# Optimization experiments

Hardware: AMD Instinct MI355X
Metric: run time of the kernel (lower is better)

## Reference

```python
import jax, jax.numpy as jnp
import numpy as np
import math

B, N, D = 8, 4096, 1024
H = 8          # num_heads
NC = 2         # n_classes


def setup_inputs() -> dict:
    key = jax.random.key(0)
    ks = jax.random.split(key, 12)
    s = 1.0 / math.sqrt(D)
    return {
        "inputs": jax.random.normal(ks[0], (B, N, D), jnp.float32),
        # enc: Linear(D, 1) + Sigmoid
        "W_enc": jax.random.normal(ks[1], (1, D), jnp.float32) * s,
        "b_enc": jnp.zeros((1,), jnp.float32),
        "cls_token": jax.random.normal(ks[2], (1, 1, D), jnp.float32) * s,
        # depthwise Conv2d(D, D, 3, padding=1, groups=D)
        "conv_w": jax.random.normal(ks[3], (D, 1, 3, 3), jnp.float32) * 0.1,
        "conv_b": jnp.zeros((D,), jnp.float32),
        # MAB projections (torch Linear weight layout [out, in])
        "Wq": jax.random.normal(ks[4], (D, D), jnp.float32) * s,
        "bq": jnp.zeros((D,), jnp.float32),
        "Wk": jax.random.normal(ks[5], (D, D), jnp.float32) * s,
        "bk": jnp.zeros((D,), jnp.float32),
        "Wv": jax.random.normal(ks[6], (D, D), jnp.float32) * s,
        "bv": jnp.zeros((D,), jnp.float32),
        "Wo": jax.random.normal(ks[7], (D, D), jnp.float32) * s,
        "bo": jnp.zeros((D,), jnp.float32),
        # final classifier Linear(D, NC)
        "Wfc": jax.random.normal(ks[8], (NC, D), jnp.float32) * s,
        "bfc": jnp.zeros((NC,), jnp.float32),
    }


def reference(inputs, W_enc, b_enc, cls_token, conv_w, conv_b,
              Wq, bq, Wk, bk, Wv, bv, Wo, bo, Wfc, bfc):
    b, n, d = inputs.shape
    # ---- recalib(option='max', k=1): top-1 instance per bag as query ----
    a1 = jax.nn.sigmoid(inputs @ W_enc.T + b_enc)[..., 0]            # [B, N]
    idx = jnp.argmax(a1, axis=1)                                      # [B]
    Q = jnp.take_along_axis(inputs, idx[:, None, None], axis=1)       # [B, 1, D]
    # ---- shift_feature ----
    inputs = jax.nn.relu(inputs - Q)
    # ---- pad to square grid, prepend cls token ----
    _H = int(np.ceil(np.sqrt(n)))
    add = _H * _H - n
    x = jnp.concatenate([inputs, inputs[:, :add, :]], axis=1)         # [B, _H*_H, D]
    cls = jnp.broadcast_to(cls_token, (b, 1, d))
    x = jnp.concatenate([cls, x], axis=1)                             # [B, S, D]
    cls_tok, feat = x[:, 0], x[:, 1:]
    # ---- depthwise conv residual on the 2D grid ----
    cnn = feat.transpose(0, 2, 1).reshape(b, d, _H, _H)               # [B, C, H, W]
    conv = jax.lax.conv_general_dilated(
        cnn, conv_w, window_strides=(1, 1), padding='SAME',
        dimension_numbers=('NCHW', 'OIHW', 'NCHW'),
        feature_group_count=d) + conv_b[None, :, None, None]
    cnn = conv + cnn
    xf = cnn.reshape(b, d, _H * _H).transpose(0, 2, 1)
    x = jnp.concatenate([cls_tok[:, None, :], xf], axis=1)            # [B, S, D]
    # ---- MAB(Q, x): manual multi-head attention ----
    Qp = Q @ Wq.T + bq                                                # [B, 1, D]
    K = x @ Wk.T + bk                                                 # [B, S, D]
    V = x @ Wv.T + bv
    dh = d // H
    qh = Qp.reshape(b, 1, H, dh).transpose(0, 2, 1, 3)                # [B, H, 1, dh]
    kh = K.reshape(b, -1, H, dh).transpose(0, 2, 1, 3)                # [B, H, S, dh]
    vh = V.reshape(b, -1, H, dh).transpose(0, 2, 1, 3)
    # NOTE: original scales by sqrt(dim_V), not sqrt(d_head)
    logits = jnp.einsum('bhqd,bhkd->bhqk', qh, kh) / jnp.asarray(math.sqrt(d), jnp.float32)
    A = jax.nn.softmax(logits, axis=-1)
    oh = qh + jnp.einsum('bhqk,bhkd->bhqd', A, vh)                    # residual inside heads
    O = oh.transpose(0, 2, 1, 3).reshape(b, 1, d)                     # [B, 1, D]
    O = O + jax.nn.relu(O @ Wo.T + bo)
    bag = O[:, 0]                                                     # [B, D]
    out = bag @ Wfc.T + bfc                                           # [B, NC]
    return out
```

## Files before the change

kernel.cpp:

```cpp
#include <hip/hip_runtime.h>
#include <hip/hip_bf16.h>


#define NTOK 4096
#define DD 1024

#define FO_ARG 0
#define FO_S1  16
#define FO_CWT 4160
#define FO_QP  13376
#define FO_W   21568
#define FO_MS  87232
#define FO_YP  95424
#define FO_Y   4289728
#define FO_O1  4355264
#define FO_O2  4363456
#define FO_AW  4371648
#define FO_XF  8388608

#define LSTRIDE 101

__global__ void k_init(const float* __restrict__ convw, float* __restrict__ cwT) {
  int gid = blockIdx.x * 256 + threadIdx.x;
  if (gid < 9216) {
    int d = gid / 9, p = gid - d * 9;
    cwT[p * DD + d] = convw[gid];
  }
}

__global__ void k_argmax1(const float* __restrict__ inp, const float* __restrict__ Wenc,
                          const float* __restrict__ benc, unsigned long long* __restrict__ s1buf) {
  __shared__ unsigned long long lb[4];
  int wave = threadIdx.x >> 6, lane = threadIdx.x & 63;
  int b = blockIdx.x >> 8;
  int r0 = ((blockIdx.x & 255) << 4) + (wave << 2);
  const float4* base = (const float4*)(inp + ((size_t)b * NTOK + r0) * DD);
  const float4* wp = (const float4*)Wenc;
  float s0 = 0.f, s1 = 0.f, s2 = 0.f, s3 = 0.f;
#pragma unroll
  for (int k = 0; k < 4; ++k) {
    int off = lane + (k << 6);
    float4 w4 = wp[off];
    float4 a0 = base[off];
    float4 a1 = base[256 + off];
    float4 a2 = base[512 + off];
    float4 a3 = base[768 + off];
    s0 = fmaf(w4.x, a0.x, s0); s0 = fmaf(w4.y, a0.y, s0); s0 = fmaf(w4.z, a0.z, s0); s0 = fmaf(w4.w, a0.w, s0);
    s1 = fmaf(w4.x, a1.x, s1); s1 = fmaf(w4.y, a1.y, s1); s1 = fmaf(w4.z, a1.z, s1); s1 = fmaf(w4.w, a1.w, s1);
    s2 = fmaf(w4.x, a2.x, s2); s2 = fmaf(w4.y, a2.y, s2); s2 = fmaf(w4.z, a2.z, s2); s2 = fmaf(w4.w, a2.w, s2);
    s3 = fmaf(w4.x, a3.x, s3); s3 = fmaf(w4.y, a3.y, s3); s3 = fmaf(w4.z, a3.z, s3); s3 = fmaf(w4.w, a3.w, s3);
  }
#pragma unroll
  for (int mk = 32; mk >= 1; mk >>= 1) {
    s0 += __shfl_xor(s0, mk); s1 += __shfl_xor(s1, mk);
    s2 += __shfl_xor(s2, mk); s3 += __shfl_xor(s3, mk);
  }
  if (lane == 0) {
    float be = benc[0];
    float v[4] = {s0 + be, s1 + be, s2 + be, s3 + be};
    unsigned long long bst = 0ull;
#pragma unroll
    for (int i = 0; i < 4; ++i) {
      unsigned u = __float_as_uint(v[i]);
      u = (u & 0x80000000u) ? ~u : (u | 0x80000000u);
      unsigned long long p = ((unsigned long long)u << 32) |
                             (unsigned long long)(0xFFFFFFFFu - (unsigned)(r0 + i));
      bst = bst > p ? bst : p;
    }
    lb[wave] = bst;
  }
  __syncthreads();
  if (threadIdx.x == 0) {
    unsigned long long m = lb[0];
#pragma unroll
    for (int i = 1; i < 4; ++i) m = m > lb[i] ? m : lb[i];
    s1buf[blockIdx.x] = m;
  }
}

__global__ void k_argmax2(const unsigned long long* __restrict__ s1buf,
                          unsigned long long* __restrict__ argbest) {
  __shared__ unsigned long long red[256];
  int tid = threadIdx.x, b = blockIdx.x;
  red[tid] = s1buf[b * 256 + tid];
  __syncthreads();
  for (int s = 128; s > 0; s >>= 1) {
    if (tid < s) { unsigned long long o = red[tid + s]; if (o > red[tid]) red[tid] = o; }
    __syncthreads();
  }
  if (tid == 0) argbest[b] = red[0];
}

__global__ void k_qp(const float* __restrict__ inp, const float* __restrict__ Wq,
                     const float* __restrict__ bq, const unsigned long long* __restrict__ argbest,
                     float* __restrict__ Qp) {
  int wave = threadIdx.x >> 6, lane = threadIdx.x & 63;
  int b = blockIdx.x >> 8;
  int i = ((blockIdx.x & 255) << 2) + wave;
  unsigned idx = 0xFFFFFFFFu - (unsigned)(argbest[b] & 0xFFFFFFFFull);
  const float4* qr = (const float4*)(inp + ((size_t)b * NTOK + idx) * DD);
  const float4* wr = (const float4*)(Wq + (size_t)i * DD);
  float s = 0.f;
#pragma unroll
  for (int k = 0; k < 4; ++k) {
    float4 a = wr[lane + (k << 6)], x = qr[lane + (k << 6)];
    s = fmaf(a.x, x.x, s); s = fmaf(a.y, x.y, s);
    s = fmaf(a.z, x.z, s); s = fmaf(a.w, x.w, s);
  }
  for (int m = 32; m > 0; m >>= 1) s += __shfl_xor(s, m);
  if (lane == 0) Qp[b * DD + i] = s + bq[i];
}

__global__ void k_w(const float* __restrict__ Wk, const float* __restrict__ Qp,
                    float* __restrict__ wbuf) {
  __shared__ float qs[1024];
  __shared__ float sred[2048];
  const int tid = threadIdx.x;
  const int h = blockIdx.x >> 5, jb = blockIdx.x & 31;
  {
    int b = tid >> 5, i4 = tid & 31;
    ((float4*)qs)[b * 32 + i4] = ((const float4*)Qp)[b * 256 + (h << 5) + i4];
  }
  __syncthreads();
  const int jl = tid & 31, ig = tid >> 5;
  const float* wkp = Wk + (size_t)((h << 7) + (ig << 4)) * DD + (jb << 5) + jl;
  float acc[8];
#pragma unroll
  for (int b = 0; b < 8; ++b) acc[b] = 0.f;
#pragma unroll
  for (int ii = 0; ii < 16; ++ii) {
    float wv = wkp[(size_t)ii * DD];
    int i = (ig << 4) + ii;
#pragma unroll
    for (int b = 0; b < 8; ++b) acc[b] = fmaf(qs[(b << 7) + i], wv, acc[b]);
  }
#pragma unroll
  for (int b = 0; b < 8; ++b) sred[ig * 256 + (b << 5) + jl] = acc[b];
  __syncthreads();
  {
    int b = tid >> 5, j2 = tid & 31;
    float s = 0.f;
#pragma unroll
    for (int g = 0; g < 8; ++g) s += sred[g * 256 + (b << 5) + j2];
    wbuf[(size_t)((b << 3) + h) * DD + (jb << 5) + j2] = s;
  }
}

__global__ __launch_bounds__(512, 4) void k_logits(
    const float* __restrict__ inp, const float* __restrict__ convb,
    const float* __restrict__ cwT, const float* __restrict__ wbuf,
    const unsigned long long* __restrict__ argbest,
    float* __restrict__ plog, float* __restrict__ xf) {
  __shared__ float4 sred4[32 * LSTRIDE];
  const int tid = threadIdx.x, bx = blockIdx.x;
  const int b = bx >> 9, tile = (bx >> 3) & 63, cidx = bx & 7;
  const int R0 = (tile >> 3) << 3, C0 = (tile & 7) << 3;
  const unsigned idxq = 0xFFFFFFFFu - (unsigned)(argbest[b] & 0xFFFFFFFFull);
  const float* inpb = inp + (size_t)b * NTOK * DD;
  const float* qrow = inpb + (size_t)idxq * DD;
  const int gg = tid & 31, ts = tid >> 5;
  const int jg = tid >> 5, rq = (tid >> 3) & 3, ca = tid & 7;
  const int r0a = rq << 1;
  const int jc = cidx << 7;

  float acc[2][8];
#pragma unroll
  for (int i = 0; i < 2; ++i)
#pragma unroll
    for (int h = 0; h < 8; ++h) acc[i][h] = 0.f;
  float4 xs0[2], xs1[2];

  {
    const int js = jc + (gg << 2);
    float4 qv = *(const float4*)(qrow + js);
    for (int t = ts; t < 100; t += 16) {
      int tr = t / 10, tc = t - tr * 10;
      int gr = R0 - 1 + tr, gc = C0 - 1 + tc;
      float4 v = make_float4(0.f, 0.f, 0.f, 0.f);
      if (gr >= 0 && gr < 64 && gc >= 0 && gc < 64) {
        float4 rv = *(const float4*)(inpb + (size_t)((gr << 6) + gc) * DD + js);
        v.x = fmaxf(rv.x - qv.x, 0.f); v.y = fmaxf(rv.y - qv.y, 0.f);
        v.z = fmaxf(rv.z - qv.z, 0.f); v.w = fmaxf(rv.w - qv.w, 0.f);
      }
      sred4[gg * LSTRIDE + t] = v;
    }
  }
  __syncthreads();
#pragma unroll
  for (int sub = 0; sub < 2; ++sub) {
    const int g = (sub << 4) + jg;
    const int j4 = jc + (g << 2);
    float4 cwr[9];
#pragma unroll
    for (int p = 0; p < 9; ++p) cwr[p] = *(const float4*)(cwT + p * DD + j4);
    float4 cb4 = *(const float4*)(convb + j4);
    const float4* fb = sred4 + g * LSTRIDE;
    float4 x0 = cb4, x1 = cb4;
    {
      float4 rw[4][3];
#pragma unroll
      for (int rr = 0; rr < 4; ++rr)
#pragma unroll
        for (int dc = 0; dc < 3; ++dc)
          rw[rr][dc] = fb[(r0a + rr) * 10 + ca + dc];
#pragma unroll
      for (int dr = 0; dr < 3; ++dr)
#pragma unroll
        for (int dc = 0; dc < 3; ++dc) {
          float4 w = cwr[dr * 3 + dc];
          float4 f0 = rw[dr][dc], f1 = rw[dr + 1][dc];
          x0.x = fmaf(w.x, f0.x, x0.x); x0.y = fmaf(w.y, f0.y, x0.y);
          x0.z = fmaf(w.z, f0.z, x0.z); x0.w = fmaf(w.w, f0.w, x0.w);
          x1.x = fmaf(w.x, f1.x, x1.x); x1.y = fmaf(w.y, f1.y, x1.y);
          x1.z = fmaf(w.z, f1.z, x1.z); x1.w = fmaf(w.w, f1.w, x1.w);
        }
      x0.x += rw[1][1].x; x0.y += rw[1][1].y; x0.z += rw[1][1].z; x0.w += rw[1][1].w;
      x1.x += rw[2][1].x; x1.y += rw[2][1].y; x1.z += rw[2][1].z; x1.w += rw[2][1].w;
    }
    xs0[sub] = x0; xs1[sub] = x1;
#pragma unroll
    for (int h = 0; h < 8; ++h) {
      float4 whv = *(const float4*)(wbuf + (size_t)(b * 8 + h) * DD + j4);
      float a0 = acc[0][h], a1 = acc[1][h];
      a0 = fmaf(whv.x, x0.x, a0); a0 = fmaf(whv.y, x0.y, a0);
      a0 = fmaf(whv.z, x0.z, a0); a0 = fmaf(whv.w, x0.w, a0);
      a1 = fmaf(whv.x, x1.x, a1); a1 = fmaf(whv.y, x1.y, a1);
      a1 = fmaf(whv.z, x1.z, a1); a1 = fmaf(whv.w, x1.w, a1);
      acc[0][h] = a0; acc[1][h] = a1;
    }
  }
  __syncthreads();
  float* red = (float*)sred4;
#pragma unroll
  for (int it = 0; it < 2; ++it)
#pragma unroll
    for (int h = 0; h < 8; ++h)
      red[jg * 512 + ((r0a + it) * 8 + ca) * 8 + h] = acc[it][h];
  __syncthreads();
  {
    float s = 0.f;
#pragma unroll
    for (int g = 0; g < 16; ++g) s += red[g * 512 + tid];
    plog[(size_t)bx * 512 + tid] = s;
  }
  __syncthreads();
  float4* ldsx = sred4;
  {
    const int tk0 = (r0a << 3) + ca;
#pragma unroll
    for (int sub = 0; sub < 2; ++sub) {
      int q = (sub << 4) + jg;
      ldsx[tk0 * 33 + q] = xs0[sub];
      ldsx[(tk0 + 8) * 33 + q] = xs1[sub];
    }
  }
  __syncthreads();
  {
    float* xfb = xf + (size_t)((b << 6) + tile) * (64 * DD) + jc;
#pragma unroll
    for (int it = 0; it < 4; ++it) {
      int idx = (it << 9) + tid;
      int tk = idx >> 5, q = idx & 31;
      float4 v = ldsx[tk * 33 + q];
      *(float4*)(xfb + (size_t)tk * DD + (q << 2)) = v;
    }
  }
}

__global__ void k_sm(const float* __restrict__ plog, float* __restrict__ aw,
                     float2* __restrict__ msbuf) {
  __shared__ float atile[512];
  const int tid = threadIdx.x, bt = blockIdx.x;
  const float* pp = plog + (size_t)bt * 8 * 512;
  float s0 = 0.f, s1 = 0.f;
#pragma unroll
  for (int c = 0; c < 8; ++c) {
    s0 += pp[c * 512 + tid];
    s1 += pp[c * 512 + 256 + tid];
  }
  {
    int o = tid, h = o & 7, tok = o >> 3;
    atile[h * 64 + tok] = s0 * 0.03125f;
    o = tid + 256; h = o & 7; tok = o >> 3;
    atile[h * 64 + tok] = s1 * 0.03125f;
  }
  __syncthreads();
  const int hh = tid >> 5, sl = tid & 31;
  float l1 = atile[hh * 64 + sl], l2 = atile[hh * 64 + 32 + sl];
  float mx = fmaxf(l1, l2);
#pragma unroll
  for (int mk = 16; mk >= 1; mk >>= 1) mx = fmaxf(mx, __shfl_xor(mx, mk));
  float e1 = __expf(l1 - mx), e2 = __expf(l2 - mx);
  float Ssum = e1 + e2;
#pragma unroll
  for (int mk = 16; mk >= 1; mk >>= 1) Ssum += __shfl_xor(Ssum, mk);
  aw[(size_t)bt * 512 + sl * 8 + hh] = e1;
  aw[(size_t)bt * 512 + (32 + sl) * 8 + hh] = e2;
  if (sl == 0) {
    int b = bt >> 6, tile = bt & 63;
    msbuf[((b << 3) + hh) * 64 + tile] = make_float2(mx, Ssum);
  }
}

__global__ __launch_bounds__(512, 8) void k_ysum(
    const float* __restrict__ xf, const float* __restrict__ aw,
    float* __restrict__ ypart) {
  __shared__ float atile[512];
  const int tid = threadIdx.x, bt = blockIdx.x;
  atile[tid] = aw[(size_t)bt * 512 + tid];
  __syncthreads();
  const float* xbase = xf + (size_t)bt * (64 * DD) + (tid << 1);
  float2 acc[8];
#pragma unroll
  for (int h = 0; h < 8; ++h) acc[h] = make_float2(0.f, 0.f);
#pragma unroll 4
  for (int t = 0; t < 64; ++t) {
    float2 v = *(const float2*)(xbase + (size_t)t * DD);
    float4 aA = *(const float4*)&atile[t * 8];
    float4 aB = *(const float4*)&atile[t * 8 + 4];
    acc[0].x = fmaf(aA.x, v.x, acc[0].x); acc[0].y = fmaf(aA.x, v.y, acc[0].y);
    acc[1].x = fmaf(aA.y, v.x, acc[1].x); acc[1].y = fmaf(aA.y, v.y, acc[1].y);
    acc[2].x = fmaf(aA.z, v.x, acc[2].x); acc[2].y = fmaf(aA.z, v.y, acc[2].y);
    acc[3].x = fmaf(aA.w, v.x, acc[3].x); acc[3].y = fmaf(aA.w, v.y, acc[3].y);
    acc[4].x = fmaf(aB.x, v.x, acc[4].x); acc[4].y = fmaf(aB.x, v.y, acc[4].y);
    acc[5].x = fmaf(aB.y, v.x, acc[5].x); acc[5].y = fmaf(aB.y, v.y, acc[5].y);
    acc[6].x = fmaf(aB.z, v.x, acc[6].x); acc[6].y = fmaf(aB.z, v.y, acc[6].y);
    acc[7].x = fmaf(aB.w, v.x, acc[7].x); acc[7].y = fmaf(aB.w, v.y, acc[7].y);
  }
  const int b = bt >> 6, tile = bt & 63;
#pragma unroll
  for (int h = 0; h < 8; ++h)
    *(float2*)(ypart + ((size_t)((b * 8 + h) * 64 + tile)) * DD + (tid << 1)) = acc[h];
}

__global__ void k_comb(const float2* __restrict__ msbuf, const float* __restrict__ wbuf,
                       const float* __restrict__ cls, const float* __restrict__ ypart,
                       float* __restrict__ ybuf) {
  __shared__ float redl[256];
  __shared__ float wgt[64];
  __shared__ float wclss;
  __shared__ float4 sacc[256];
  int tid = threadIdx.x;
  int bh = blockIdx.x >> 3, cs = blockIdx.x & 7;
  {
    float4 a = ((const float4*)(wbuf + (size_t)bh * DD))[tid];
    float4 c = ((const float4*)cls)[tid];
    redl[tid] = a.x * c.x + a.y * c.y + a.z * c.z + a.w * c.w;
  }
  __syncthreads();
  for (int s = 128; s > 0; s >>= 1) { if (tid < s) redl[tid] += redl[tid + s]; __syncthreads(); }
  float l0 = redl[0] * 0.03125f;
  if (tid < 64) {
    float2 ms = msbuf[bh * 64 + tid];
    float m = ms.x, S = ms.y;
    float M = m;
#pragma unroll
    for (int mk = 32; mk >= 1; mk >>= 1) M = fmaxf(M, __shfl_xor(M, mk));
    M = fmaxf(M, l0);
    float w = __expf(m - M);
    float z = S * w;
#pragma unroll
    for (int mk = 32; mk >= 1; mk >>= 1) z += __shfl_xor(z, mk);
    float ec = __expf(l0 - M);
    float Z = z + ec;
    wgt[tid] = w / Z;
    if (tid == 0) wclss = ec / Z;
  }
  __syncthreads();
  int ch4 = (cs << 5) + (tid & 31);
  int tg = tid >> 5;
  const float* yp = ypart + (size_t)bh * 64 * DD + (ch4 << 2);
  float4 acc = make_float4(0.f, 0.f, 0.f, 0.f);
#pragma unroll
  for (int tt = 0; tt < 8; ++tt) {
    int t = tg * 8 + tt;
    float w = wgt[t];
    float4 v = *(const float4*)(yp + (size_t)t * DD);
    acc.x = fmaf(w, v.x, acc.x); acc.y = fmaf(w, v.y, acc.y);
    acc.z = fmaf(w, v.z, acc.z); acc.w = fmaf(w, v.w, acc.w);
  }
  sacc[tg * 32 + (tid & 31)] = acc;
  __syncthreads();
  if (tid < 32) {
    int c4 = (cs << 5) + tid;
    float4 s = sacc[tid];
#pragma unroll
    for (int g = 1; g < 8; ++g) {
      float4 v = sacc[g * 32 + tid];
      s.x += v.x; s.y += v.y; s.z += v.z; s.w += v.w;
    }
    float wc = wclss;
    float4 cv = *(const float4*)(cls + (c4 << 2));
    s.x = fmaf(wc, cv.x, s.x); s.y = fmaf(wc, cv.y, s.y);
    s.z = fmaf(wc, cv.z, s.z); s.w = fmaf(wc, cv.w, s.w);
    *(float4*)(ybuf + (size_t)bh * DD + (c4 << 2)) = s;
  }
}

__global__ void k_o1(const float* __restrict__ Wv, const float* __restrict__ bv,
                     const float* __restrict__ Qp, const float* __restrict__ ybuf,
                     float* __restrict__ O1) {
  int wave = threadIdx.x >> 6, lane = threadIdx.x & 63;
  int b = blockIdx.x >> 8;
  int i = ((blockIdx.x & 255) << 2) + wave;
  int h = i >> 7;
  const float4* wr = (const float4*)(Wv + (size_t)i * DD);
  const float4* yr = (const float4*)(ybuf + (size_t)(b * 8 + h) * DD);
  float s = 0.f;
#pragma unroll
  for (int k = 0; k < 4; ++k) {
    float4 a = wr[lane + (k << 6)], x = yr[lane + (k << 6)];
    s = fmaf(a.x, x.x, s); s = fmaf(a.y, x.y, s);
    s = fmaf(a.z, x.z, s); s = fmaf(a.w, x.w, s);
  }
  for (int m = 32; m > 0; m >>= 1) s += __shfl_xor(s, m);
  if (lane == 0) O1[b * DD + i] = Qp[b * DD + i] + bv[i] + s;
}

__global__ void k_o2(const float* __restrict__ Wo, const float* __restrict__ bo,
                     const float* __restrict__ O1, float* __restrict__ O2) {
  int wave = threadIdx.x >> 6, lane = threadIdx.x & 63;
  int b = blockIdx.x >> 8;
  int i = ((blockIdx.x & 255) << 2) + wave;
  const float4* wr = (const float4*)(Wo + (size_t)i * DD);
  const float4* xr = (const float4*)(O1 + (size_t)b * DD);
  float s = 0.f;
#pragma unroll
  for (int k = 0; k < 4; ++k) {
    float4 a = wr[lane + (k << 6)], x = xr[lane + (k << 6)];
    s = fmaf(a.x, x.x, s); s = fmaf(a.y, x.y, s);
    s = fmaf(a.z, x.z, s); s = fmaf(a.w, x.w, s);
  }
  for (int m = 32; m > 0; m >>= 1) s += __shfl_xor(s, m);
  if (lane == 0) O2[b * DD + i] = O1[b * DD + i] + fmaxf(s + bo[i], 0.f);
}

__global__ void k_out(const float* __restrict__ Wfc, const float* __restrict__ bfc,
                      const float* __restrict__ O2, float* __restrict__ out) {
  int wave = threadIdx.x >> 6, lane = threadIdx.x & 63;
  for (int p = wave; p < 16; p += 4) {
    int b = p >> 1, cc = p & 1;
    const float4* o = (const float4*)(O2 + (size_t)b * DD);
    const float4* wr = (const float4*)(Wfc + (size_t)cc * DD);
    float s = 0.f;
#pragma unroll
    for (int k = 0; k < 4; ++k) {
      float4 a = o[lane + (k << 6)], x = wr[lane + (k << 6)];
      s = fmaf(a.x, x.x, s); s = fmaf(a.y, x.y, s);
      s = fmaf(a.z, x.z, s); s = fmaf(a.w, x.w, s);
    }
    for (int m = 32; m > 0; m >>= 1) s += __shfl_xor(s, m);
    if (lane == 0) out[p] = s + bfc[cc];
  }
}

extern "C" void kernel_launch(void* const* d_in, const int* in_sizes, int n_in,
                              void* d_out, int out_size, void* d_ws, size_t ws_size,
                              hipStream_t stream) {
  const float* inp   = (const float*)d_in[0];
  const float* Wenc  = (const float*)d_in[1];
  const float* benc  = (const float*)d_in[2];
  const float* cls   = (const float*)d_in[3];
  const float* convw = (const float*)d_in[4];
  const float* convb = (const float*)d_in[5];
  const float* Wq    = (const float*)d_in[6];
  const float* bq    = (const float*)d_in[7];
  const float* Wk    = (const float*)d_in[8];
  const float* bv    = (const float*)d_in[11];
  const float* Wv    = (const float*)d_in[10];
  const float* Wo    = (const float*)d_in[12];
  const float* bo    = (const float*)d_in[13];
  const float* Wfc   = (const float*)d_in[14];
  const float* bfc   = (const float*)d_in[15];
  float* out = (float*)d_out;
  float* W = (float*)d_ws;
  unsigned long long* argbest = (unsigned long long*)(W + FO_ARG);
  unsigned long long* s1buf   = (unsigned long long*)(W + FO_S1);
  float* cwT   = W + FO_CWT;
  float* Qp    = W + FO_QP;
  float* wbuf  = W + FO_W;
  float2* msbuf = (float2*)(W + FO_MS);
  float* ypart = W + FO_YP;
  float* plog  = W + FO_YP;
  float* aw    = W + FO_AW;
  float* xf    = W + FO_XF;
  float* ybuf  = W + FO_Y;
  float* O1    = W + FO_O1;
  float* O2    = W + FO_O2;

  hipLaunchKernelGGL(k_init,    dim3(36),   dim3(256), 0, stream, convw, cwT);
  hipLaunchKernelGGL(k_argmax1, dim3(2048), dim3(256), 0, stream, inp, Wenc, benc, s1buf);
  hipLaunchKernelGGL(k_argmax2, dim3(8),    dim3(256), 0, stream, s1buf, argbest);
  hipLaunchKernelGGL(k_qp,      dim3(2048), dim3(256), 0, stream, inp, Wq, bq, argbest, Qp);
  hipLaunchKernelGGL(k_w,       dim3(256),  dim3(256), 0, stream, Wk, Qp, wbuf);
  hipLaunchKernelGGL(k_logits,  dim3(4096), dim3(512), 0, stream, inp, convb, cwT, wbuf, argbest, plog, xf);
  hipLaunchKernelGGL(k_sm,      dim3(512),  dim3(256), 0, stream, plog, aw, msbuf);
  hipLaunchKernelGGL(k_ysum,    dim3(512),  dim3(512), 0, stream, xf, aw, ypart);
  hipLaunchKernelGGL(k_comb,    dim3(512),  dim3(256), 0, stream, msbuf, wbuf, cls, ypart, ybuf);
  hipLaunchKernelGGL(k_o1,      dim3(2048), dim3(256), 0, stream, Wv, bv, Qp, ybuf, O1);
  hipLaunchKernelGGL(k_o2,      dim3(2048), dim3(256), 0, stream, Wo, bo, O1, O2);
  hipLaunchKernelGGL(k_out,     dim3(1),    dim3(256), 0, stream, Wfc, bfc, O2, out);
}
```

Measured before the change: 358.3 us.

## Split logits kernel into narrower channel chunks and fuse softmax into ysum

The logits/conv kernel now has each block handle 64 channels instead of 128, which doubles the grid to 8192 blocks and halves per-thread registers and LDS use. The separate softmax kernel is removed: k_ysum now reduces the 16 partial logit slices, computes the per-tile softmax max and sum, and keeps the exp weights in LDS, so the aw buffer round trip and one launch go away. In exchange, the partial-logit buffer doubles in size and moves to a new workspace offset. The halo load per block is also repeated for twice as many blocks.

```diff
diff --git a/kernel.cpp b/kernel.cpp
--- a/kernel.cpp
+++ b/kernel.cpp
@@ -15,8 +15,8 @@
 #define FO_Y   4289728
 #define FO_O1  4355264
 #define FO_O2  4363456
-#define FO_AW  4371648
 #define FO_XF  8388608
+#define FO_PL  41943040
 
 #define LSTRIDE 101
 
@@ -151,29 +151,29 @@
     const float* __restrict__ cwT, const float* __restrict__ wbuf,
     const unsigned long long* __restrict__ argbest,
     float* __restrict__ plog, float* __restrict__ xf) {
-  __shared__ float4 sred4[32 * LSTRIDE];
+  __shared__ float4 sred4[2048];
   const int tid = threadIdx.x, bx = blockIdx.x;
-  const int b = bx >> 9, tile = (bx >> 3) & 63, cidx = bx & 7;
+  const int b = bx >> 10, tile = (bx >> 4) & 63, cidx = bx & 15;
   const int R0 = (tile >> 3) << 3, C0 = (tile & 7) << 3;
   const unsigned idxq = 0xFFFFFFFFu - (unsigned)(argbest[b] & 0xFFFFFFFFull);
   const float* inpb = inp + (size_t)b * NTOK * DD;
   const float* qrow = inpb + (size_t)idxq * DD;
-  const int gg = tid & 31, ts = tid >> 5;
+  const int gg = tid & 15, ts = tid >> 4;
   const int jg = tid >> 5, rq = (tid >> 3) & 3, ca = tid & 7;
   const int r0a = rq << 1;
-  const int jc = cidx << 7;
+  const int jc = cidx << 6;
 
   float acc[2][8];
 #pragma unroll
   for (int i = 0; i < 2; ++i)
 #pragma unroll
     for (int h = 0; h < 8; ++h) acc[i][h] = 0.f;
-  float4 xs0[2], xs1[2];
+  float4 xs0, xs1;
 
   {
     const int js = jc + (gg << 2);
     float4 qv = *(const float4*)(qrow + js);
-    for (int t = ts; t < 100; t += 16) {
+    for (int t = ts; t < 100; t += 32) {
       int tr = t / 10, tc = t - tr * 10;
       int gr = R0 - 1 + tr, gc = C0 - 1 + tc;
       float4 v = make_float4(0.f, 0.f, 0.f, 0.f);
@@ -186,15 +186,13 @@
     }
   }
   __syncthreads();
-#pragma unroll
-  for (int sub = 0; sub < 2; ++sub) {
-    const int g = (sub << 4) + jg;
-    const int j4 = jc + (g << 2);
+  {
+    const int j4 = jc + (jg << 2);
     float4 cwr[9];
 #pragma unroll
     for (int p = 0; p < 9; ++p) cwr[p] = *(const float4*)(cwT + p * DD + j4);
     float4 cb4 = *(const float4*)(convb + j4);
-    const float4* fb = sred4 + g * LSTRIDE;
+    const float4* fb = sred4 + jg * LSTRIDE;
     float4 x0 = cb4, x1 = cb4;
     {
       float4 rw[4][3];
@@ -217,7 +215,7 @@
       x0.x += rw[1][1].x; x0.y += rw[1][1].y; x0.z += rw[1][1].z; x0.w += rw[1][1].w;
       x1.x += rw[2][1].x; x1.y += rw[2][1].y; x1.z += rw[2][1].z; x1.w += rw[2][1].w;
     }
-    xs0[sub] = x0; xs1[sub] = x1;
+    xs0 = x0; xs1 = x1;
 #pragma unroll
     for (int h = 0; h < 8; ++h) {
       float4 whv = *(const float4*)(wbuf + (size_t)(b * 8 + h) * DD + j4);
@@ -247,67 +245,52 @@
   float4* ldsx = sred4;
   {
     const int tk0 = (r0a << 3) + ca;
-#pragma unroll
-    for (int sub = 0; sub < 2; ++sub) {
-      int q = (sub << 4) + jg;
-      ldsx[tk0 * 33 + q] = xs0[sub];
-      ldsx[(tk0 + 8) * 33 + q] = xs1[sub];
-    }
+    ldsx[tk0 * 17 + jg] = xs0;
+    ldsx[(tk0 + 8) * 17 + jg] = xs1;
   }
   __syncthreads();
   {
     float* xfb = xf + (size_t)((b << 6) + tile) * (64 * DD) + jc;
 #pragma unroll
-    for (int it = 0; it < 4; ++it) {
+    for (int it = 0; it < 2; ++it) {
       int idx = (it << 9) + tid;
-      int tk = idx >> 5, q = idx & 31;
-      float4 v = ldsx[tk * 33 + q];
+      int tk = idx >> 4, q = idx & 15;
+      float4 v = ldsx[tk * 17 + q];
       *(float4*)(xfb + (size_t)tk * DD + (q << 2)) = v;
     }
   }
 }
 
-__global__ void k_sm(const float* __restrict__ plog, float* __restrict__ aw,
-                     float2* __restrict__ msbuf) {
+__global__ __launch_bounds__(512, 8) void k_ysum(
+    const float* __restrict__ plog, const float* __restrict__ xf,
+    float2* __restrict__ msbuf, float* __restrict__ ypart) {
   __shared__ float atile[512];
   const int tid = threadIdx.x, bt = blockIdx.x;
-  const float* pp = plog + (size_t)bt * 8 * 512;
-  float s0 = 0.f, s1 = 0.f;
-#pragma unroll
-  for (int c = 0; c < 8; ++c) {
-    s0 += pp[c * 512 + tid];
-    s1 += pp[c * 512 + 256 + tid];
-  }
-  {
-    int o = tid, h = o & 7, tok = o >> 3;
-    atile[h * 64 + tok] = s0 * 0.03125f;
-    o = tid + 256; h = o & 7; tok = o >> 3;
-    atile[h * 64 + tok] = s1 * 0.03125f;
-  }
-  __syncthreads();
-  const int hh = tid >> 5, sl = tid & 31;
-  float l1 = atile[hh * 64 + sl], l2 = atile[hh * 64 + 32 + sl];
-  float mx = fmaxf(l1, l2);
-#pragma unroll
-  for (int mk = 16; mk >= 1; mk >>= 1) mx = fmaxf(mx, __shfl_xor(mx, mk));
-  float e1 = __expf(l1 - mx), e2 = __expf(l2 - mx);
-  float Ssum = e1 + e2;
-#pragma unroll
-  for (int mk = 16; mk >= 1; mk >>= 1) Ssum += __shfl_xor(Ssum, mk);
-  aw[(size_t)bt * 512 + sl * 8 + hh] = e1;
-  aw[(size_t)bt * 512 + (32 + sl) * 8 + hh] = e2;
-  if (sl == 0) {
-    int b = bt >> 6, tile = bt & 63;
-    msbuf[((b << 3) + hh) * 64 + tile] = make_float2(mx, Ssum);
-  }
-}
-
-__global__ __launch_bounds__(512, 8) void k_ysum(
-    const float* __restrict__ xf, const float* __restrict__ aw,
-    float* __restrict__ ypart) {
-  __shared__ float atile[512];
-  const int tid = threadIdx.x, bt = blockIdx.x;
-  atile[tid] = aw[(size_t)bt * 512 + tid];
+  {
+    const float* pp = plog + (size_t)bt * 16 * 512;
+    float s = 0.f;
+#pragma unroll
+    for (int c = 0; c < 16; ++c) s += pp[c * 512 + tid];
+    atile[tid] = s * 0.03125f;
+  }
+  __syncthreads();
+  {
+    const int w = tid >> 6, l = tid & 63;
+    float v = atile[l * 8 + w];
+    float mx = v;
+#pragma unroll
+    for (int mk = 32; mk >= 1; mk >>= 1) mx = fmaxf(mx, __shfl_xor(mx, mk));
+    float e = __expf(v - mx);
+    float Ss = e;
+#pragma unroll
+    for (int mk = 32; mk >= 1; mk >>= 1) Ss += __shfl_xor(Ss, mk);
+    __syncthreads();
+    atile[l * 8 + w] = e;
+    if (l == 0) {
+      int b = bt >> 6, tile = bt & 63;
+      msbuf[((b << 3) + w) * 64 + tile] = make_float2(mx, Ss);
+    }
+  }
   __syncthreads();
   const float* xbase = xf + (size_t)bt * (64 * DD) + (tid << 1);
   float2 acc[8];
@@ -481,8 +464,7 @@
   float* wbuf  = W + FO_W;
   float2* msbuf = (float2*)(W + FO_MS);
   float* ypart = W + FO_YP;
-  float* plog  = W + FO_YP;
-  float* aw    = W + FO_AW;
+  float* plog  = W + FO_PL;
   float* xf    = W + FO_XF;
   float* ybuf  = W + FO_Y;
   float* O1    = W + FO_O1;
@@ -493,9 +475,8 @@
   hipLaunchKernelGGL(k_argmax2, dim3(8),    dim3(256), 0, stream, s1buf, argbest);
   hipLaunchKernelGGL(k_qp,      dim3(2048), dim3(256), 0, stream, inp, Wq, bq, argbest, Qp);
   hipLaunchKernelGGL(k_w,       dim3(256),  dim3(256), 0, stream, Wk, Qp, wbuf);
-  hipLaunchKernelGGL(k_logits,  dim3(4096), dim3(512), 0, stream, inp, convb, cwT, wbuf, argbest, plog, xf);
-  hipLaunchKernelGGL(k_sm,      dim3(512),  dim3(256), 0, stream, plog, aw, msbuf);
-  hipLaunchKernelGGL(k_ysum,    dim3(512),  dim3(512), 0, stream, xf, aw, ypart);
+  hipLaunchKernelGGL(k_logits,  dim3(8192), dim3(512), 0, stream, inp, convb, cwT, wbuf, argbest, plog, xf);
+  hipLaunchKernelGGL(k_ysum,    dim3(512),  dim3(512), 0, stream, plog, xf, msbuf, ypart);
   hipLaunchKernelGGL(k_comb,    dim3(512),  dim3(256), 0, stream, msbuf, wbuf, cls, ypart, ybuf);
   hipLaunchKernelGGL(k_o1,      dim3(2048), dim3(256), 0, stream, Wv, bv, Qp, ybuf, O1);
   hipLaunchKernelGGL(k_o2,      dim3(2048), dim3(256), 0, stream, Wo, bo, O1, O2);
```

Result: faster. 344.0 us (-4.0%).
